# Optimization experiments

Measured on AMD Instinct MI355X. Metric: run time of the kernel, lower is better.

## Reference

```python
import jax, jax.numpy as jnp
import numpy as np

BATCH = 16384
NNZ = 524288
INPUT_DIM = 30000
OUTPUT_DIM = 300


def setup_inputs() -> dict:
    key = jax.random.key(0)
    k1, k2, k3, k4 = jax.random.split(key, 4)
    sp_rows = jnp.sort(jax.random.randint(k1, (NNZ,), 0, BATCH, dtype=jnp.int32))
    sp_cols = jax.random.randint(k2, (NNZ,), 0, INPUT_DIM, dtype=jnp.int32)
    sp_vals = jax.random.uniform(k3, (NNZ,), dtype=jnp.float32)
    # glorot init for weights, zeros bias (as in the TF module)
    scale = jnp.sqrt(6.0 / (INPUT_DIM + OUTPUT_DIM)).astype(jnp.float32)
    weights = jax.random.uniform(k4, (INPUT_DIM, OUTPUT_DIM), dtype=jnp.float32,
                                 minval=-scale, maxval=scale)
    bias = jnp.zeros((OUTPUT_DIM,), dtype=jnp.float32)
    return {"sp_rows": sp_rows, "sp_cols": sp_cols, "sp_vals": sp_vals,
            "weights": weights, "bias": bias, "batch_size": BATCH}


def reference(sp_rows, sp_cols, sp_vals, weights, bias, batch_size):
    # sparse [batch, input_dim] @ dense [input_dim, output_dim]:
    # gather weight rows per nnz, scale by value, segment-sum into output rows.
    contrib = sp_vals[:, None] * weights[sp_cols]          # [nnz, output_dim]
    dense_vector = jax.ops.segment_sum(contrib, sp_rows,
                                       num_segments=batch_size)  # [batch, output_dim]
    dense_vector = dense_vector + bias
    return jax.nn.relu(dense_vector)
```

## Files before the change

### kernel.cpp

```cpp
#include <hip/hip_runtime.h>

#define OUT_DIM 300

typedef _Float16 half2_t __attribute__((ext_vector_type(2)));
typedef _Float16 half8_t __attribute__((ext_vector_type(8)));

__global__ __launch_bounds__(256) void setup4_kernel(
    const int* __restrict__ rows, int* __restrict__ row_ptr,
    const float* __restrict__ w, unsigned char* __restrict__ wf,
    int nnz, int batch, int in_dim, int scat_blocks)
{
    if ((int)blockIdx.x < scat_blocks) {
        int i = blockIdx.x * 256 + threadIdx.x;
        if (i >= nnz) return;
        int r = rows[i];
        int prev = (i == 0) ? -1 : rows[i - 1];
        for (int q = prev + 1; q <= r; ++q) row_ptr[q] = i;
        if (i == nnz - 1)
            for (int q = r + 1; q <= batch; ++q) row_ptr[q] = nnz;
        return;
    }
    const int UPR = OUT_DIM / 2;
    int j = ((int)blockIdx.x - scat_blocks) * 256 + threadIdx.x;
    if (j >= in_dim * UPR) return;
    int r = j / UPR;
    int k = j - r * UPR;
    int s = k / 40; if (s > 3) s = 3;
    int kc = k - 40 * s;
    float2 f = *(const float2*)(w + (size_t)r * OUT_DIM + 2 * k);
    half2_t h;
    h.x = (_Float16)f.x;
    h.y = (_Float16)f.y;
    *(half2_t*)(wf + ((size_t)s * in_dim + r) * 160 + kc * 4) = h;
}

__global__ __launch_bounds__(256) void spmm4w(
    const int* __restrict__ row_ptr,
    const int* __restrict__ cols,
    const float* __restrict__ vals,
    const unsigned char* __restrict__ wf,
    const float* __restrict__ bias,
    float* __restrict__ out,
    int batch, int in_dim)
{
    __shared__ uint2 sh[4][76];

    const int slice = blockIdx.x & 3;
    const int wave  = threadIdx.x >> 6;
    const int lane  = threadIdx.x & 63;
    const int row   = (blockIdx.x >> 2) * 4 + wave;
    if (row >= batch) return;

    const int grp = lane / 10;
    const int ch  = lane - grp * 10;
    const int choff = ch * 16;

    const unsigned char* wslice = wf + (size_t)slice * in_dim * 160;
    uint2* shw = sh[wave];

    if (lane < 12) shw[64 + lane] = make_uint2(0u, 0u);

    const int lo = row_ptr[row];
    const int hi = row_ptr[row + 1];

    float a0 = 0.f, a1 = 0.f, a2 = 0.f, a3 = 0.f;
    float a4 = 0.f, a5 = 0.f, a6 = 0.f, a7 = 0.f;

    for (int base = lo; base < hi; base += 64) {
        const int rem = hi - base;
        const int cnt = rem < 64 ? rem : 64;

        uint2 ov = make_uint2(0u, 0u);
        if (lane < cnt) {
            ov.x = (unsigned)(cols[base + lane] * 160);
            ov.y = __float_as_uint(vals[base + lane]);
        }
        shw[lane] = ov;

        const int rr  = (cnt + 5) / 6;
        const int rrp = (rr + 3) & ~3;
        for (int r0 = 0; r0 < rrp; r0 += 4) {
#pragma unroll
            for (int u = 0; u < 4; ++u) {
                uint2 q = shw[6 * (r0 + u) + grp];
                float v = __uint_as_float(q.y);
                half8_t wv = *(const half8_t*)(wslice + q.x + choff);
                a0 += v * (float)wv[0];
                a1 += v * (float)wv[1];
                a2 += v * (float)wv[2];
                a3 += v * (float)wv[3];
                a4 += v * (float)wv[4];
                a5 += v * (float)wv[5];
                a6 += v * (float)wv[6];
                a7 += v * (float)wv[7];
            }
        }
    }

    a0 += __shfl_down(a0, 30); a1 += __shfl_down(a1, 30);
    a2 += __shfl_down(a2, 30); a3 += __shfl_down(a3, 30);
    a4 += __shfl_down(a4, 30); a5 += __shfl_down(a5, 30);
    a6 += __shfl_down(a6, 30); a7 += __shfl_down(a7, 30);

    float f0 = a0 + __shfl_down(a0, 10) + __shfl_down(a0, 20);
    float f1 = a1 + __shfl_down(a1, 10) + __shfl_down(a1, 20);
    float f2 = a2 + __shfl_down(a2, 10) + __shfl_down(a2, 20);
    float f3 = a3 + __shfl_down(a3, 10) + __shfl_down(a3, 20);
    float f4 = a4 + __shfl_down(a4, 10) + __shfl_down(a4, 20);
    float f5 = a5 + __shfl_down(a5, 10) + __shfl_down(a5, 20);
    float f6 = a6 + __shfl_down(a6, 10) + __shfl_down(a6, 20);
    float f7 = a7 + __shfl_down(a7, 10) + __shfl_down(a7, 20);

    const int nlan = (slice == 3) ? 8 : 10;
    if (lane < nlan) {
        const int col = slice * 80 + lane * 8;
        float* orow = out + (size_t)row * OUT_DIM + col;
        const float4 b0 = *(const float4*)(bias + col);
        float4 s0;
        s0.x = fmaxf(f0 + b0.x, 0.f);
        s0.y = fmaxf(f1 + b0.y, 0.f);
        s0.z = fmaxf(f2 + b0.z, 0.f);
        s0.w = fmaxf(f3 + b0.w, 0.f);
        *(float4*)orow = s0;
        if (slice < 3 || lane < 7) {
            const float4 b1 = *(const float4*)(bias + col + 4);
            float4 s1;
            s1.x = fmaxf(f4 + b1.x, 0.f);
            s1.y = fmaxf(f5 + b1.y, 0.f);
            s1.z = fmaxf(f6 + b1.z, 0.f);
            s1.w = fmaxf(f7 + b1.w, 0.f);
            *(float4*)(orow + 4) = s1;
        }
    }
}

__global__ __launch_bounds__(256) void row_ptr_scatter(
    const int* __restrict__ rows, int* __restrict__ row_ptr, int nnz, int batch)
{
    int i = blockIdx.x * 256 + threadIdx.x;
    if (i >= nnz) return;
    int r = rows[i];
    int prev = (i == 0) ? -1 : rows[i - 1];
    for (int q = prev + 1; q <= r; ++q) row_ptr[q] = i;
    if (i == nnz - 1)
        for (int q = r + 1; q <= batch; ++q) row_ptr[q] = nnz;
}

__global__ __launch_bounds__(256) void spmm_wave_f32_kernel(
    const int* __restrict__ row_ptr,
    const int* __restrict__ cols,
    const float* __restrict__ vals,
    const float* __restrict__ weights,
    const float* __restrict__ bias,
    float* __restrict__ out,
    int batch)
{
    const int wave = threadIdx.x >> 6;
    const int lane = threadIdx.x & 63;
    const int row  = blockIdx.x * 4 + wave;
    if (row >= batch) return;

    const int lo = row_ptr[row];
    const int hi = row_ptr[row + 1];
    float4 acc0 = make_float4(0.f, 0.f, 0.f, 0.f);
    float4 acc1 = make_float4(0.f, 0.f, 0.f, 0.f);
    const bool tail = (lane < 75 - 64);

    for (int base = lo; base < hi; base += 64) {
        const int rem = hi - base;
        const int cnt = rem < 64 ? rem : 64;
        int   c = 0;
        float v = 0.0f;
        if (lane < cnt) { c = cols[base + lane]; v = vals[base + lane]; }
        const int rounds = (cnt + 7) & ~7;
        for (int k = 0; k < rounds; k += 8) {
#pragma unroll
            for (int u = 0; u < 8; ++u) {
                const int   cc = __shfl(c, k + u);
                const float vv = __shfl(v, k + u);
                const float4* wrow = (const float4*)(weights + (size_t)cc * OUT_DIM);
                float4 w0 = wrow[lane];
                acc0.x += vv * w0.x; acc0.y += vv * w0.y;
                acc0.z += vv * w0.z; acc0.w += vv * w0.w;
                if (tail) {
                    float4 w1 = wrow[64 + lane];
                    acc1.x += vv * w1.x; acc1.y += vv * w1.y;
                    acc1.z += vv * w1.z; acc1.w += vv * w1.w;
                }
            }
        }
    }

    const float4* b4 = (const float4*)bias;
    float4* orow = (float4*)(out + (size_t)row * OUT_DIM);
    float4 b0 = b4[lane];
    float4 r0;
    r0.x = fmaxf(acc0.x + b0.x, 0.f);
    r0.y = fmaxf(acc0.y + b0.y, 0.f);
    r0.z = fmaxf(acc0.z + b0.z, 0.f);
    r0.w = fmaxf(acc0.w + b0.w, 0.f);
    orow[lane] = r0;
    if (tail) {
        float4 b1 = b4[64 + lane];
        float4 r1;
        r1.x = fmaxf(acc1.x + b1.x, 0.f);
        r1.y = fmaxf(acc1.y + b1.y, 0.f);
        r1.z = fmaxf(acc1.z + b1.z, 0.f);
        r1.w = fmaxf(acc1.w + b1.w, 0.f);
        orow[64 + lane] = r1;
    }
}

extern "C" void kernel_launch(void* const* d_in, const int* in_sizes, int n_in,
                              void* d_out, int out_size, void* d_ws, size_t ws_size,
                              hipStream_t stream) {
    const int*   sp_rows = (const int*)d_in[0];
    const int*   sp_cols = (const int*)d_in[1];
    const float* sp_vals = (const float*)d_in[2];
    const float* weights = (const float*)d_in[3];
    const float* bias    = (const float*)d_in[4];
    float* out = (float*)d_out;

    const int nnz    = in_sizes[0];
    const int w_elts = in_sizes[3];
    const int in_dim = w_elts / OUT_DIM;
    const int batch  = out_size / OUT_DIM;

    size_t rp_bytes = (size_t)(batch + 1) * sizeof(int);
    size_t wf_off   = (rp_bytes + 255) & ~(size_t)255;
    size_t need4    = wf_off + (size_t)in_dim * 4 * 160 + 256;

    int* row_ptr = (int*)d_ws;
    const int rowgroups = (batch + 3) / 4;

    if (ws_size >= need4) {
        unsigned char* wf = (unsigned char*)d_ws + wf_off;
        const int scat_blocks = (nnz + 255) / 256;
        const int rep_blocks  = (in_dim * (OUT_DIM / 2) + 255) / 256;
        setup4_kernel<<<scat_blocks + rep_blocks, 256, 0, stream>>>(
            sp_rows, row_ptr, weights, wf, nnz, batch, in_dim, scat_blocks);
        spmm4w<<<rowgroups * 4, 256, 0, stream>>>(
            row_ptr, sp_cols, sp_vals, wf, bias, out, batch, in_dim);
    } else {
        row_ptr_scatter<<<(nnz + 255) / 256, 256, 0, stream>>>(
            sp_rows, row_ptr, nnz, batch);
        spmm_wave_f32_kernel<<<(batch + 3) / 4, 256, 0, stream>>>(
            row_ptr, sp_cols, sp_vals, weights, bias, out, batch);
    }
}
```

Baseline: 137.5 us.

## Process four rows per wave with shared nnz staging and vectorize weight repack

The SpMM kernel now assigns four consecutive output rows to each wave instead of one. It stages 64-entry chunks of column offsets and values in LDS that are shared across those rows, and refills the chunk when a row crosses its end. The weight repack kernel now reads float4 and writes half4 per thread instead of float2/half2, and splits blocks by output slice. The aim is to cut per-wave launch overhead, row_ptr loads, and staging loads of short chunks. In exchange each wave runs its rows serially, which reduces parallel waves and may leave more idle padded slots per chunk.

After: 140.5 us. +2.1%, slower.

```diff
diff --git a/kernel.cpp b/kernel.cpp
--- a/kernel.cpp
+++ b/kernel.cpp
@@ -2,10 +2,10 @@
 
 #define OUT_DIM 300
 
-typedef _Float16 half2_t __attribute__((ext_vector_type(2)));
+typedef _Float16 half4_t __attribute__((ext_vector_type(4)));
 typedef _Float16 half8_t __attribute__((ext_vector_type(8)));
 
-__global__ __launch_bounds__(256) void setup4_kernel(
+__global__ __launch_bounds__(256) void setup4x_kernel(
     const int* __restrict__ rows, int* __restrict__ row_ptr,
     const float* __restrict__ w, unsigned char* __restrict__ wf,
     int nnz, int batch, int in_dim, int scat_blocks)
@@ -20,21 +20,21 @@
             for (int q = r + 1; q <= batch; ++q) row_ptr[q] = nnz;
         return;
     }
-    const int UPR = OUT_DIM / 2;
-    int j = ((int)blockIdx.x - scat_blocks) * 256 + threadIdx.x;
-    if (j >= in_dim * UPR) return;
-    int r = j / UPR;
-    int k = j - r * UPR;
-    int s = k / 40; if (s > 3) s = 3;
-    int kc = k - 40 * s;
-    float2 f = *(const float2*)(w + (size_t)r * OUT_DIM + 2 * k);
-    half2_t h;
-    h.x = (_Float16)f.x;
-    h.y = (_Float16)f.y;
-    *(half2_t*)(wf + ((size_t)s * in_dim + r) * 160 + kc * 4) = h;
-}
-
-__global__ __launch_bounds__(256) void spmm4w(
+    const int s  = (int)blockIdx.x & 3;
+    const int q  = ((int)blockIdx.x - scat_blocks) >> 2;
+    const int ng = (s == 3) ? 15 : 20;
+    int i = q * 256 + (int)threadIdx.x;
+    if (i >= in_dim * ng) return;
+    int r = i / ng;
+    int g = i - r * ng;
+    const float4 f = *(const float4*)(w + (size_t)r * OUT_DIM + 80 * s + 4 * g);
+    half4_t h;
+    h[0] = (_Float16)f.x; h[1] = (_Float16)f.y;
+    h[2] = (_Float16)f.z; h[3] = (_Float16)f.w;
+    *(half4_t*)(wf + ((size_t)s * in_dim + r) * 160 + g * 8) = h;
+}
+
+__global__ __launch_bounds__(256) void spmm4r(
     const int* __restrict__ row_ptr,
     const int* __restrict__ cols,
     const float* __restrict__ vals,
@@ -43,13 +43,13 @@
     float* __restrict__ out,
     int batch, int in_dim)
 {
-    __shared__ uint2 sh[4][76];
+    __shared__ uint2 sh[4][104];
 
     const int slice = blockIdx.x & 3;
     const int wave  = threadIdx.x >> 6;
     const int lane  = threadIdx.x & 63;
-    const int row   = (blockIdx.x >> 2) * 4 + wave;
-    if (row >= batch) return;
+    const int r0    = ((blockIdx.x >> 2) * 4 + wave) * 4;
+    if (r0 >= batch) return;
 
     const int grp = lane / 10;
     const int ch  = lane - grp * 10;
@@ -57,79 +57,109 @@
 
     const unsigned char* wslice = wf + (size_t)slice * in_dim * 160;
     uint2* shw = sh[wave];
-
-    if (lane < 12) shw[64 + lane] = make_uint2(0u, 0u);
-
-    const int lo = row_ptr[row];
-    const int hi = row_ptr[row + 1];
-
-    float a0 = 0.f, a1 = 0.f, a2 = 0.f, a3 = 0.f;
-    float a4 = 0.f, a5 = 0.f, a6 = 0.f, a7 = 0.f;
-
-    for (int base = lo; base < hi; base += 64) {
-        const int rem = hi - base;
-        const int cnt = rem < 64 ? rem : 64;
-
+    if (lane == 0) shw[96] = make_uint2(0u, 0u);
+
+    int rp[5];
+#pragma unroll
+    for (int i = 0; i < 5; ++i) {
+        int rr = r0 + i; if (rr > batch) rr = batch;
+        rp[i] = row_ptr[rr];
+    }
+
+    int cb = rp[0];
+    {
+        int cnt = rp[4] - cb; if (cnt > 64) cnt = 64;
         uint2 ov = make_uint2(0u, 0u);
         if (lane < cnt) {
-            ov.x = (unsigned)(cols[base + lane] * 160);
-            ov.y = __float_as_uint(vals[base + lane]);
+            ov.x = (unsigned)(cols[cb + lane] * 160);
+            ov.y = __float_as_uint(vals[cb + lane]);
         }
         shw[lane] = ov;
-
-        const int rr  = (cnt + 5) / 6;
-        const int rrp = (rr + 3) & ~3;
-        for (int r0 = 0; r0 < rrp; r0 += 4) {
-#pragma unroll
-            for (int u = 0; u < 4; ++u) {
-                uint2 q = shw[6 * (r0 + u) + grp];
-                float v = __uint_as_float(q.y);
-                half8_t wv = *(const half8_t*)(wslice + q.x + choff);
-                a0 += v * (float)wv[0];
-                a1 += v * (float)wv[1];
-                a2 += v * (float)wv[2];
-                a3 += v * (float)wv[3];
-                a4 += v * (float)wv[4];
-                a5 += v * (float)wv[5];
-                a6 += v * (float)wv[6];
-                a7 += v * (float)wv[7];
+    }
+
+#pragma unroll
+    for (int i = 0; i < 4; ++i) {
+        const int rowi = r0 + i;
+        if (rowi >= batch) break;
+        const int eR = rp[i + 1];
+        int cur = rp[i];
+
+        float a0 = 0.f, a1 = 0.f, a2 = 0.f, a3 = 0.f;
+        float a4 = 0.f, a5 = 0.f, a6 = 0.f, a7 = 0.f;
+
+        for (;;) {
+            const int s0 = cur - cb;
+            int e = eR - cb; if (e > 64) e = 64;
+            const int nr = e - s0;
+            if (nr > 0) {
+                const int rr  = (nr + 5) / 6;
+                const int rrp = (rr + 3) & ~3;
+                for (int z = 0; z < rrp; z += 4) {
+#pragma unroll
+                    for (int u = 0; u < 4; ++u) {
+                        int slot = s0 + 6 * (z + u) + grp;
+                        slot = (slot < e) ? slot : 96;
+                        uint2 qq = shw[slot];
+                        float v = __uint_as_float(qq.y);
+                        half8_t wv = *(const half8_t*)(wslice + qq.x + choff);
+                        a0 += v * (float)wv[0];
+                        a1 += v * (float)wv[1];
+                        a2 += v * (float)wv[2];
+                        a3 += v * (float)wv[3];
+                        a4 += v * (float)wv[4];
+                        a5 += v * (float)wv[5];
+                        a6 += v * (float)wv[6];
+                        a7 += v * (float)wv[7];
+                    }
+                }
             }
-        }
-    }
-
-    a0 += __shfl_down(a0, 30); a1 += __shfl_down(a1, 30);
-    a2 += __shfl_down(a2, 30); a3 += __shfl_down(a3, 30);
-    a4 += __shfl_down(a4, 30); a5 += __shfl_down(a5, 30);
-    a6 += __shfl_down(a6, 30); a7 += __shfl_down(a7, 30);
-
-    float f0 = a0 + __shfl_down(a0, 10) + __shfl_down(a0, 20);
-    float f1 = a1 + __shfl_down(a1, 10) + __shfl_down(a1, 20);
-    float f2 = a2 + __shfl_down(a2, 10) + __shfl_down(a2, 20);
-    float f3 = a3 + __shfl_down(a3, 10) + __shfl_down(a3, 20);
-    float f4 = a4 + __shfl_down(a4, 10) + __shfl_down(a4, 20);
-    float f5 = a5 + __shfl_down(a5, 10) + __shfl_down(a5, 20);
-    float f6 = a6 + __shfl_down(a6, 10) + __shfl_down(a6, 20);
-    float f7 = a7 + __shfl_down(a7, 10) + __shfl_down(a7, 20);
-
-    const int nlan = (slice == 3) ? 8 : 10;
-    if (lane < nlan) {
-        const int col = slice * 80 + lane * 8;
-        float* orow = out + (size_t)row * OUT_DIM + col;
-        const float4 b0 = *(const float4*)(bias + col);
-        float4 s0;
-        s0.x = fmaxf(f0 + b0.x, 0.f);
-        s0.y = fmaxf(f1 + b0.y, 0.f);
-        s0.z = fmaxf(f2 + b0.z, 0.f);
-        s0.w = fmaxf(f3 + b0.w, 0.f);
-        *(float4*)orow = s0;
-        if (slice < 3 || lane < 7) {
-            const float4 b1 = *(const float4*)(bias + col + 4);
-            float4 s1;
-            s1.x = fmaxf(f4 + b1.x, 0.f);
-            s1.y = fmaxf(f5 + b1.y, 0.f);
-            s1.z = fmaxf(f6 + b1.z, 0.f);
-            s1.w = fmaxf(f7 + b1.w, 0.f);
-            *(float4*)(orow + 4) = s1;
+            if (eR > cb + 64) {
+                cb += 64;
+                int cnt = rp[4] - cb; if (cnt > 64) cnt = 64;
+                uint2 ov = make_uint2(0u, 0u);
+                if (lane < cnt) {
+                    ov.x = (unsigned)(cols[cb + lane] * 160);
+                    ov.y = __float_as_uint(vals[cb + lane]);
+                }
+                shw[lane] = ov;
+                cur = cb;
+            } else break;
+        }
+
+        a0 += __shfl_down(a0, 30); a1 += __shfl_down(a1, 30);
+        a2 += __shfl_down(a2, 30); a3 += __shfl_down(a3, 30);
+        a4 += __shfl_down(a4, 30); a5 += __shfl_down(a5, 30);
+        a6 += __shfl_down(a6, 30); a7 += __shfl_down(a7, 30);
+
+        float f0 = a0 + __shfl_down(a0, 10) + __shfl_down(a0, 20);
+        float f1 = a1 + __shfl_down(a1, 10) + __shfl_down(a1, 20);
+        float f2 = a2 + __shfl_down(a2, 10) + __shfl_down(a2, 20);
+        float f3 = a3 + __shfl_down(a3, 10) + __shfl_down(a3, 20);
+        float f4 = a4 + __shfl_down(a4, 10) + __shfl_down(a4, 20);
+        float f5 = a5 + __shfl_down(a5, 10) + __shfl_down(a5, 20);
+        float f6 = a6 + __shfl_down(a6, 10) + __shfl_down(a6, 20);
+        float f7 = a7 + __shfl_down(a7, 10) + __shfl_down(a7, 20);
+
+        const int nlan = (slice == 3) ? 8 : 10;
+        if (lane < nlan) {
+            const int col = slice * 80 + lane * 8;
+            float* orow = out + (size_t)rowi * OUT_DIM + col;
+            const float4 b0 = *(const float4*)(bias + col);
+            float4 s0v;
+            s0v.x = fmaxf(f0 + b0.x, 0.f);
+            s0v.y = fmaxf(f1 + b0.y, 0.f);
+            s0v.z = fmaxf(f2 + b0.z, 0.f);
+            s0v.w = fmaxf(f3 + b0.w, 0.f);
+            *(float4*)orow = s0v;
+            if (slice < 3 || lane < 7) {
+                const float4 b1 = *(const float4*)(bias + col + 4);
+                float4 s1v;
+                s1v.x = fmaxf(f4 + b1.x, 0.f);
+                s1v.y = fmaxf(f5 + b1.y, 0.f);
+                s1v.z = fmaxf(f6 + b1.z, 0.f);
+                s1v.w = fmaxf(f7 + b1.w, 0.f);
+                *(float4*)(orow + 4) = s1v;
+            }
         }
     }
 }
@@ -231,15 +261,15 @@
     size_t need4    = wf_off + (size_t)in_dim * 4 * 160 + 256;
 
     int* row_ptr = (int*)d_ws;
-    const int rowgroups = (batch + 3) / 4;
 
     if (ws_size >= need4) {
         unsigned char* wf = (unsigned char*)d_ws + wf_off;
         const int scat_blocks = (nnz + 255) / 256;
-        const int rep_blocks  = (in_dim * (OUT_DIM / 2) + 255) / 256;
-        setup4_kernel<<<scat_blocks + rep_blocks, 256, 0, stream>>>(
+        const int bps = (in_dim * 20 + 255) / 256;
+        setup4x_kernel<<<scat_blocks + 4 * bps, 256, 0, stream>>>(
             sp_rows, row_ptr, weights, wf, nnz, batch, in_dim, scat_blocks);
-        spmm4w<<<rowgroups * 4, 256, 0, stream>>>(
+        const int rowblocks16 = (batch + 15) / 16;
+        spmm4r<<<rowblocks16 * 4, 256, 0, stream>>>(
             row_ptr, sp_cols, sp_vals, wf, bias, out, batch, in_dim);
     } else {
         row_ptr_scatter<<<(nnz + 255) / 256, 256, 0, stream>>>(
```
